# Optimization experiments

Hardware: AMD Instinct MI355X
Metric: run time of the kernel (lower is better)

The kernel has to match this reference:

```python
import jax, jax.numpy as jnp
import numpy as np

NUM_NODES = 2048
EMB = (512, 512, 256)
LATENT = 512
N_FEAT = 512
N_TOTAL = 16384  # batch_size * NUM_NODES
N_EDGES = 524288


def setup_inputs() -> dict:
    key = jax.random.key(0)
    ks = jax.random.split(key, 14)
    s = 0.02
    inp = {
        "x": jax.random.normal(ks[0], (N_TOTAL, N_FEAT), jnp.float32),
        "edge_index": jax.random.randint(ks[1], (2, N_EDGES), 0, N_TOTAL, dtype=jnp.int64),
        "batch_size": 8,
        "batch_index": jax.random.randint(ks[2], (N_TOTAL,), 0, 8, dtype=jnp.int64),
        "W1": jax.random.normal(ks[3], (N_FEAT, EMB[0]), jnp.float32) * s,
        "b1": jnp.zeros((EMB[0],), jnp.float32),
        "W2": jax.random.normal(ks[4], (EMB[0], EMB[1]), jnp.float32) * s,
        "b2": jnp.zeros((EMB[1],), jnp.float32),
        "W3": jax.random.normal(ks[5], (EMB[1], EMB[2]), jnp.float32) * s,
        "b3": jnp.zeros((EMB[2],), jnp.float32),
        "We": jax.random.normal(ks[6], (NUM_NODES * EMB[2], LATENT), jnp.float32) * s,
        "be": jnp.zeros((LATENT,), jnp.float32),
        "Wd": jax.random.normal(ks[7], (LATENT, NUM_NODES), jnp.float32) * s,
        "bd": jnp.zeros((NUM_NODES,), jnp.float32),
    }
    return inp


def reference(x, edge_index, batch_size, batch_index, W1, b1, W2, b2, W3, b3, We, be, Wd, bd):
    N = x.shape[0]
    loops = jnp.arange(N)
    row = jnp.concatenate([edge_index[0], loops])  # sources
    col = jnp.concatenate([edge_index[1], loops])  # targets
    # symmetric degree normalization (PyG GCNConv with self loops)
    deg = jax.ops.segment_sum(jnp.ones_like(col, dtype=x.dtype), col, num_segments=N)
    dinv = jnp.where(deg > 0, jax.lax.rsqrt(deg), jnp.zeros_like(deg))
    norm = (dinv[row] * dinv[col])[:, None]  # [E+N, 1]

    def gcn(h, W, b):
        h = h @ W  # transform first (PyG order)
        return jax.ops.segment_sum(h[row] * norm, col, num_segments=N) + b

    h = jax.nn.relu(gcn(x, W1, b1))
    h = jax.nn.relu(gcn(h, W2, b2))
    h = gcn(h, W3, b3)                      # [N, EMB[2]]
    h = h.reshape(-1, NUM_NODES * EMB[2])   # [batch, NUM_NODES*EMB[2]]
    z = h @ We + be                          # encoder Linear
    out = z @ Wd + bd                        # decoder Linear -> [batch, NUM_NODES]
    return out
```

## Files before the change

kernel.cpp:

```cpp
#include <hip/hip_runtime.h>
#include <stdint.h>

#define NT 16384
#define NN 2048
#define NB 8
#define NBKT 16

typedef __attribute__((ext_vector_type(4))) float f32x4;
typedef __attribute__((ext_vector_type(8))) short s16x8;
typedef __attribute__((ext_vector_type(4))) short s16x4;

__device__ __forceinline__ float bf2f(short u) {
    unsigned v = ((unsigned)(unsigned short)u) << 16;
    return __builtin_bit_cast(float, v);
}
__device__ __forceinline__ short f2bf(float f) {
    unsigned u = __builtin_bit_cast(unsigned, f);
    u += 0x7fffu + ((u >> 16) & 1u);
    return (short)(u >> 16);
}
__device__ __forceinline__ void gload16(const void* g, void* l) {
    __builtin_amdgcn_global_load_lds(
        (const __attribute__((address_space(1))) void*)g,
        (__attribute__((address_space(3))) void*)l, 16, 0, 0);
}
__device__ __forceinline__ long long eidx(const void* ei, long long i, int is64) {
    if (is64) return ((const long long*)ei)[i];
    return (long long)((const int*)ei)[i];
}

__global__ void k_init(const void* ei, int* flag, int* cnt16) {
    if (blockIdx.x == 64) {
        __shared__ int bad;
        if (threadIdx.x == 0) bad = 0;
        __syncthreads();
        const long long* p = (const long long*)ei;
        for (int i = threadIdx.x; i < 2048; i += 256) {
            long long v = p[i];
            if (v < 0 || v >= NT) bad = 1;
        }
        __syncthreads();
        if (threadIdx.x == 0) *flag = bad ? 0 : 1;
    } else {
        int base = blockIdx.x * 4096 + threadIdx.x;
#pragma unroll
        for (int q = 0; q < 16; q++) cnt16[base + q * 256] = 0;
    }
}

__global__ void k_count16(const void* ei, int E, const int* flag, int* cnt16) {
    int e = blockIdx.x * 256 + threadIdx.x;
    if (e >= E) return;
    int f = *flag;
    int r = (int)eidx(ei, e, f);
    int c = (int)eidx(ei, (long long)E + e, f);
    atomicAdd(&cnt16[c * NBKT + (r >> 10)], 1);
}

__global__ void k_deg(const int* __restrict__ cnt16, int* __restrict__ deg) {
    int n = blockIdx.x * 256 + threadIdx.x;
    const int* p = cnt16 + n * NBKT;
    int s = 0;
#pragma unroll
    for (int j = 0; j < NBKT; j++) s += p[j];
    deg[n] = s;
}

__global__ __launch_bounds__(1024) void k_scan(const int* __restrict__ count,
        int* __restrict__ offs, float* __restrict__ dinv) {
    __shared__ int ps[1024];
    const int t = threadIdx.x;
    const int base = t * 16;
    int loc[16];
    int s = 0;
#pragma unroll
    for (int j = 0; j < 16; j++) { loc[j] = count[base + j]; s += loc[j]; }
    ps[t] = s;
    __syncthreads();
    for (int o = 1; o < 1024; o <<= 1) {
        int v = (t >= o) ? ps[t - o] : 0;
        __syncthreads();
        ps[t] += v;
        __syncthreads();
    }
    int ex = ps[t] - s;
#pragma unroll
    for (int j = 0; j < 16; j++) {
        offs[base + j] = ex;
        ex += loc[j];
        dinv[base + j] = rsqrtf((float)(loc[j] + 1));
    }
}

__global__ void k_bcur(const int* __restrict__ cnt16, const int* __restrict__ offs,
                       int* __restrict__ bcur) {
    int n = blockIdx.x * 256 + threadIdx.x;
    int running = offs[n];
#pragma unroll
    for (int b = 0; b < NBKT; b++) {
        bcur[n * NBKT + b] = running;
        running += cnt16[n * NBKT + b];
    }
}

__global__ void k_fill16(const void* ei, int E, const int* flag,
                         int* bcur, int* csr) {
    int e = blockIdx.x * 256 + threadIdx.x;
    if (e >= E) return;
    int f = *flag;
    int r = (int)eidx(ei, e, f);
    int c = (int)eidx(ei, (long long)E + e, f);
    int pos = atomicAdd(&bcur[c * NBKT + (r >> 10)], 1);
    csr[pos] = r;
}

__global__ void k_convscale(const float* __restrict__ W1, const float* __restrict__ W2,
                            const float* __restrict__ W3, short* __restrict__ Wt1,
                            short* __restrict__ Wt2, short* __restrict__ Wt3,
                            const float* __restrict__ x, const float* __restrict__ dinv,
                            short* __restrict__ xs) {
    if (blockIdx.x < 8192) {
        int i = blockIdx.x * 256 + threadIdx.x;
        f32x4 v = *(const f32x4*)(x + (size_t)i * 4);
        float d = dinv[i >> 7];
        s16x4 o;
#pragma unroll
        for (int j = 0; j < 4; j++) o[j] = f2bf(v[j] * d);
        *(s16x4*)(xs + (size_t)i * 4) = o;
    } else {
        int idx = (blockIdx.x - 8192) * 256 + threadIdx.x;
        const float* W; short* Wt; int N, base;
        if (idx < 262144)      { W = W1; Wt = Wt1; N = 512; base = idx; }
        else if (idx < 524288) { W = W2; Wt = Wt2; N = 512; base = idx - 262144; }
        else                   { W = W3; Wt = Wt3; N = 256; base = idx - 524288; }
        int k = base / N, n = base - k * N;
        Wt[(size_t)n * 512 + k] = f2bf(W[base]);
    }
}

__global__ __launch_bounds__(256, 4) void k_gemm(const short* __restrict__ A,
        const short* __restrict__ Bt, short* __restrict__ Co, int N, int K) {
    __shared__ short As[64 * 64];
    __shared__ short Bs[128 * 64];
    const int t = threadIdx.x;
    const int w = t >> 6, l = t & 63;
    const int row0 = blockIdx.x * 64;
    const int col0 = blockIdx.y * 128;
    const int lr = l & 15, lhi = l >> 4;
    const int wc = w * 32;
    f32x4 acc[4][2] = {};
    int arow[2], ajs[2], brow[4], bjs[4];
#pragma unroll
    for (int i = 0; i < 2; i++) {
        int s = t + i * 256;
        arow[i] = s >> 3; ajs[i] = (s & 7) ^ (arow[i] & 7);
    }
#pragma unroll
    for (int i = 0; i < 4; i++) {
        int s = t + i * 256;
        brow[i] = s >> 3; bjs[i] = (s & 7) ^ (brow[i] & 7);
    }
    int aoff[2][4], boff[2][2];
#pragma unroll
    for (int kk = 0; kk < 2; kk++) {
#pragma unroll
        for (int m = 0; m < 4; m++) {
            int ar = m * 16 + lr;
            aoff[kk][m] = ar * 64 + (((kk * 4 + lhi) ^ (ar & 7)) << 3);
        }
#pragma unroll
        for (int n = 0; n < 2; n++) {
            int br = wc + n * 16 + lr;
            boff[kk][n] = br * 64 + (((kk * 4 + lhi) ^ (br & 7)) << 3);
        }
    }
    for (int k0 = 0; k0 < K; k0 += 64) {
#pragma unroll
        for (int i = 0; i < 2; i++)
            gload16(A + (size_t)(row0 + arow[i]) * K + k0 + ajs[i] * 8,
                    (void*)(As + (t + i * 256) * 8));
#pragma unroll
        for (int i = 0; i < 4; i++)
            gload16(Bt + (size_t)(col0 + brow[i]) * K + k0 + bjs[i] * 8,
                    (void*)(Bs + (t + i * 256) * 8));
        __syncthreads();
#pragma unroll
        for (int kk = 0; kk < 2; kk++) {
            s16x8 af[4], bfr[2];
#pragma unroll
            for (int m = 0; m < 4; m++) af[m]  = *(const s16x8*)(As + aoff[kk][m]);
#pragma unroll
            for (int n = 0; n < 2; n++) bfr[n] = *(const s16x8*)(Bs + boff[kk][n]);
#pragma unroll
            for (int m = 0; m < 4; m++)
#pragma unroll
                for (int n = 0; n < 2; n++)
                    acc[m][n] = __builtin_amdgcn_mfma_f32_16x16x32_bf16(af[m], bfr[n], acc[m][n], 0, 0, 0);
        }
        __syncthreads();
    }
#pragma unroll
    for (int m = 0; m < 4; m++)
#pragma unroll
        for (int n = 0; n < 2; n++)
#pragma unroll
            for (int j = 0; j < 4; j++) {
                int r = row0 + m * 16 + lhi * 4 + j;
                int c = col0 + wc + n * 16 + lr;
                Co[(size_t)r * N + c] = f2bf(acc[m][n][j]);
            }
}

__global__ __launch_bounds__(256) void k_agg512(const short* __restrict__ T,
        const int* __restrict__ offs, const int* __restrict__ cnt,
        const int* __restrict__ csr, const float* __restrict__ dinv,
        const float* __restrict__ bias, short* __restrict__ H) {
    const int w = threadIdx.x >> 6, l = threadIdx.x & 63;
    const int node = blockIdx.x * 4 + w;
    const int c0 = l * 8;
    const short* base = T + c0;
    float acc[8];
    {
        s16x8 r = *(const s16x8*)(base + (size_t)node * 512);
#pragma unroll
        for (int v = 0; v < 8; v++) acc[v] = bf2f(r[v]);
    }
    const int beg = offs[node], end = beg + cnt[node];
    int j = beg;
    for (; j + 8 <= end; j += 8) {
        int sIx[8];
#pragma unroll
        for (int q = 0; q < 8; q++) sIx[q] = csr[j + q];
        s16x8 r[8];
#pragma unroll
        for (int q = 0; q < 8; q++) r[q] = *(const s16x8*)(base + (size_t)sIx[q] * 512);
#pragma unroll
        for (int v = 0; v < 8; v++) {
            float s01 = bf2f(r[0][v]) + bf2f(r[1][v]);
            float s23 = bf2f(r[2][v]) + bf2f(r[3][v]);
            float s45 = bf2f(r[4][v]) + bf2f(r[5][v]);
            float s67 = bf2f(r[6][v]) + bf2f(r[7][v]);
            acc[v] += (s01 + s23) + (s45 + s67);
        }
    }
    for (; j + 2 <= end; j += 2) {
        int s0 = csr[j], s1 = csr[j + 1];
        s16x8 r0 = *(const s16x8*)(base + (size_t)s0 * 512);
        s16x8 r1 = *(const s16x8*)(base + (size_t)s1 * 512);
#pragma unroll
        for (int v = 0; v < 8; v++) acc[v] += bf2f(r0[v]) + bf2f(r1[v]);
    }
    for (; j < end; j++) {
        s16x8 r0 = *(const s16x8*)(base + (size_t)csr[j] * 512);
#pragma unroll
        for (int v = 0; v < 8; v++) acc[v] += bf2f(r0[v]);
    }
    const float dc = dinv[node];
    f32x4 b0 = *(const f32x4*)(bias + c0);
    f32x4 b1 = *(const f32x4*)(bias + c0 + 4);
    s16x8 outv;
#pragma unroll
    for (int v = 0; v < 8; v++) {
        float bb = (v < 4) ? b0[v] : b1[v - 4];
        float o = acc[v] * dc + bb;
        o = fmaxf(o, 0.f);
        o *= dc;
        outv[v] = f2bf(o);
    }
    *(s16x8*)(H + (size_t)node * 512 + c0) = outv;
}

__global__ __launch_bounds__(256) void k_enc(const short* __restrict__ T,
        const int* __restrict__ offs, const int* __restrict__ cnt,
        const int* __restrict__ csr, const float* __restrict__ dinv,
        const float* __restrict__ b3, const float* __restrict__ We,
        float* __restrict__ part) {
    __shared__ float hB[8 * 512];
    __shared__ float red[32 * 128];
    const int t = threadIdx.x;
    const int w = t >> 6, l = t & 63;
    const int ln0 = blockIdx.x * 2;
    const int c0 = l * 4;
    const short* base = T + c0;
    f32x4 bb = *(const f32x4*)(b3 + c0);
    for (int p = 0; p < 4; p++) {
        const int i = w * 4 + p;
        const int b = i >> 1, lnk = i & 1;
        const int node = b * NN + ln0 + lnk;
        float acc[4];
        {
            s16x4 r = *(const s16x4*)(base + (size_t)node * 256);
#pragma unroll
            for (int v = 0; v < 4; v++) acc[v] = bf2f(r[v]);
        }
        const int beg = offs[node], end = beg + cnt[node];
        int j = beg;
        for (; j + 8 <= end; j += 8) {
            int sIx[8];
#pragma unroll
            for (int q = 0; q < 8; q++) sIx[q] = csr[j + q];
            s16x4 r[8];
#pragma unroll
            for (int q = 0; q < 8; q++) r[q] = *(const s16x4*)(base + (size_t)sIx[q] * 256);
#pragma unroll
            for (int v = 0; v < 4; v++) {
                float s01 = bf2f(r[0][v]) + bf2f(r[1][v]);
                float s23 = bf2f(r[2][v]) + bf2f(r[3][v]);
                float s45 = bf2f(r[4][v]) + bf2f(r[5][v]);
                float s67 = bf2f(r[6][v]) + bf2f(r[7][v]);
                acc[v] += (s01 + s23) + (s45 + s67);
            }
        }
        for (; j < end; j++) {
            s16x4 r0 = *(const s16x4*)(base + (size_t)csr[j] * 256);
#pragma unroll
            for (int v = 0; v < 4; v++) acc[v] += bf2f(r0[v]);
        }
        const float dc = dinv[node];
        f32x4 o;
#pragma unroll
        for (int v = 0; v < 4; v++) o[v] = acc[v] * dc + bb[v];
        *(f32x4*)(&hB[b * 512 + lnk * 256 + c0]) = o;
    }
    __syncthreads();
    const int col = (t & 127) * 4;
    const int khalf = t >> 7;
    float acc[8][4] = {};
    const float* wp = We + (size_t)(blockIdx.x * 512 + khalf * 256) * 512 + col;
    const float* hp = hB + khalf * 256;
#pragma unroll 2
    for (int k = 0; k < 256; k++) {
        f32x4 wv = *(const f32x4*)(wp + (size_t)k * 512);
        float h0 = hp[k],        h1 = hp[512 + k],  h2 = hp[1024 + k], h3v = hp[1536 + k];
        float h4 = hp[2048 + k], h5 = hp[2560 + k], h6 = hp[3072 + k], h7 = hp[3584 + k];
#pragma unroll
        for (int c = 0; c < 4; c++) {
            acc[0][c] += h0 * wv[c];
            acc[1][c] += h1 * wv[c];
            acc[2][c] += h2 * wv[c];
            acc[3][c] += h3v * wv[c];
            acc[4][c] += h4 * wv[c];
            acc[5][c] += h5 * wv[c];
            acc[6][c] += h6 * wv[c];
            acc[7][c] += h7 * wv[c];
        }
    }
    if (khalf) {
#pragma unroll
        for (int b = 0; b < 8; b++)
#pragma unroll
            for (int c = 0; c < 4; c++)
                red[(b * 4 + c) * 128 + (t - 128)] = acc[b][c];
    }
    __syncthreads();
    if (!khalf) {
#pragma unroll
        for (int b = 0; b < 8; b++) {
            f32x4 o;
#pragma unroll
            for (int c = 0; c < 4; c++) o[c] = acc[b][c] + red[(b * 4 + c) * 128 + t];
            *(f32x4*)(part + (size_t)blockIdx.x * 4096 + b * 512 + col) = o;
        }
    }
}

__global__ __launch_bounds__(256) void k_zred(const float* __restrict__ part,
                                              float* __restrict__ zpart) {
    const int n = blockIdx.x * 256 + threadIdx.x;
    const int p0 = blockIdx.y * 128;
    float s = 0.f;
    for (int q = 0; q < 128; q++) s += part[(size_t)(p0 + q) * 4096 + n];
    zpart[(size_t)blockIdx.y * 4096 + n] = s;
}

__global__ __launch_bounds__(256) void k_dec(const float* __restrict__ zpart,
        const float* __restrict__ be, const float* __restrict__ Wd,
        const float* __restrict__ bd, float* __restrict__ out) {
    __shared__ float zs[512];
    const int b = blockIdx.x >> 3;
    const int n = ((blockIdx.x & 7) << 8) + threadIdx.x;
    for (int i = threadIdx.x; i < 512; i += 256) {
        float s = be[i];
#pragma unroll
        for (int p = 0; p < 8; p++) s += zpart[(size_t)p * 4096 + b * 512 + i];
        zs[i] = s;
    }
    __syncthreads();
    float acc = bd[n];
    for (int k = 0; k < 512; k++) acc += zs[k] * Wd[(size_t)k * 2048 + n];
    out[b * 2048 + n] = acc;
}

extern "C" void kernel_launch(void* const* d_in, const int* in_sizes, int n_in,
                              void* d_out, int out_size, void* d_ws, size_t ws_size,
                              hipStream_t stream) {
    const float* x  = (const float*)d_in[0];
    const void*  ei = d_in[1];
    const float* W1 = (const float*)d_in[4];
    const float* b1 = (const float*)d_in[5];
    const float* W2 = (const float*)d_in[6];
    const float* b2 = (const float*)d_in[7];
    const float* W3 = (const float*)d_in[8];
    const float* b3 = (const float*)d_in[9];
    const float* We = (const float*)d_in[10];
    const float* be = (const float*)d_in[11];
    const float* Wd = (const float*)d_in[12];
    const float* bd = (const float*)d_in[13];
    float* out = (float*)d_out;
    const int E = in_sizes[1] / 2;

    char* ws = (char*)d_ws;
    size_t off = 0;
    auto alloc = [&](size_t bytes) {
        void* p = ws + off;
        off = (off + bytes + 255) & ~(size_t)255;
        return p;
    };
    int*   flag   = (int*)  alloc(4);
    int*   deg    = (int*)  alloc((size_t)NT * 4);
    int*   offs   = (int*)  alloc((size_t)NT * 4);
    float* dinv   = (float*)alloc((size_t)NT * 4);
    int*   csr    = (int*)  alloc((size_t)E * 4);
    short* Wt1    = (short*)alloc((size_t)512 * 512 * 2);
    short* Wt2    = (short*)alloc((size_t)512 * 512 * 2);
    short* Wt3    = (short*)alloc((size_t)256 * 512 * 2);
    short* bufA   = (short*)alloc((size_t)NT * 512 * 2);
    short* bufB   = (short*)alloc((size_t)NT * 512 * 2);
    float* part   = (float*)alloc((size_t)1024 * 4096 * 4);
    float* zpart  = (float*)alloc((size_t)8 * 4096 * 4);
    int*   cnt16  = (int*)part;
    int*   bcur   = ((int*)part) + NT * NBKT;

    k_init<<<65, 256, 0, stream>>>(ei, flag, cnt16);
    k_count16<<<(E + 255) / 256, 256, 0, stream>>>(ei, E, flag, cnt16);
    k_deg<<<NT / 256, 256, 0, stream>>>(cnt16, deg);
    k_scan<<<1, 1024, 0, stream>>>(deg, offs, dinv);
    k_bcur<<<NT / 256, 256, 0, stream>>>(cnt16, offs, bcur);
    k_fill16<<<(E + 255) / 256, 256, 0, stream>>>(ei, E, flag, bcur, csr);

    k_convscale<<<10752, 256, 0, stream>>>(W1, W2, W3, Wt1, Wt2, Wt3, x, dinv, bufA);

    dim3 g1(256, 4);
    k_gemm<<<g1, 256, 0, stream>>>(bufA, Wt1, bufB, 512, 512);
    k_agg512<<<NT / 4, 256, 0, stream>>>(bufB, offs, deg, csr, dinv, b1, bufA);
    k_gemm<<<g1, 256, 0, stream>>>(bufA, Wt2, bufB, 512, 512);
    k_agg512<<<NT / 4, 256, 0, stream>>>(bufB, offs, deg, csr, dinv, b2, bufA);
    dim3 g3(256, 2);
    k_gemm<<<g3, 256, 0, stream>>>(bufA, Wt3, bufB, 256, 512);

    k_enc<<<1024, 256, 0, stream>>>(bufB, offs, deg, csr, dinv, b3, We, part);
    dim3 gz(16, 8);
    k_zred<<<gz, 256, 0, stream>>>(part, zpart);
    k_dec<<<64, 256, 0, stream>>>(zpart, be, Wd, bd, out);
}
```

Baseline: 493.2 us.

## Split 512-wide aggregation into two 256-channel passes for cache locality

The gather-aggregate kernel now handles half the feature channels per launch, with a channel offset argument, and is launched twice per layer. Each pass touches only a 256-channel (512-byte) slice of every source row, so the gathered working set halves and more of it may stay in L2/MALL across random neighbor accesses. In exchange there are twice as many launches, the CSR indices and degrees are re-read per pass, and each lane does narrower 8-byte loads.

After: 485.0 us. No clear change (-1.7%).

```diff
diff --git a/kernel.cpp b/kernel.cpp
--- a/kernel.cpp
+++ b/kernel.cpp
@@ -211,19 +211,19 @@
             }
 }
 
-__global__ __launch_bounds__(256) void k_agg512(const short* __restrict__ T,
+__global__ __launch_bounds__(256) void k_agg512h(const short* __restrict__ T,
         const int* __restrict__ offs, const int* __restrict__ cnt,
         const int* __restrict__ csr, const float* __restrict__ dinv,
-        const float* __restrict__ bias, short* __restrict__ H) {
+        const float* __restrict__ bias, short* __restrict__ H, int choff) {
     const int w = threadIdx.x >> 6, l = threadIdx.x & 63;
     const int node = blockIdx.x * 4 + w;
-    const int c0 = l * 8;
+    const int c0 = choff + l * 4;
     const short* base = T + c0;
-    float acc[8];
+    float acc[4];
     {
-        s16x8 r = *(const s16x8*)(base + (size_t)node * 512);
-#pragma unroll
-        for (int v = 0; v < 8; v++) acc[v] = bf2f(r[v]);
+        s16x4 r = *(const s16x4*)(base + (size_t)node * 512);
+#pragma unroll
+        for (int v = 0; v < 4; v++) acc[v] = bf2f(r[v]);
     }
     const int beg = offs[node], end = beg + cnt[node];
     int j = beg;
@@ -231,11 +231,11 @@
         int sIx[8];
 #pragma unroll
         for (int q = 0; q < 8; q++) sIx[q] = csr[j + q];
-        s16x8 r[8];
-#pragma unroll
-        for (int q = 0; q < 8; q++) r[q] = *(const s16x8*)(base + (size_t)sIx[q] * 512);
-#pragma unroll
-        for (int v = 0; v < 8; v++) {
+        s16x4 r[8];
+#pragma unroll
+        for (int q = 0; q < 8; q++) r[q] = *(const s16x4*)(base + (size_t)sIx[q] * 512);
+#pragma unroll
+        for (int v = 0; v < 4; v++) {
             float s01 = bf2f(r[0][v]) + bf2f(r[1][v]);
             float s23 = bf2f(r[2][v]) + bf2f(r[3][v]);
             float s45 = bf2f(r[4][v]) + bf2f(r[5][v]);
@@ -245,29 +245,27 @@
     }
     for (; j + 2 <= end; j += 2) {
         int s0 = csr[j], s1 = csr[j + 1];
-        s16x8 r0 = *(const s16x8*)(base + (size_t)s0 * 512);
-        s16x8 r1 = *(const s16x8*)(base + (size_t)s1 * 512);
-#pragma unroll
-        for (int v = 0; v < 8; v++) acc[v] += bf2f(r0[v]) + bf2f(r1[v]);
+        s16x4 r0 = *(const s16x4*)(base + (size_t)s0 * 512);
+        s16x4 r1 = *(const s16x4*)(base + (size_t)s1 * 512);
+#pragma unroll
+        for (int v = 0; v < 4; v++) acc[v] += bf2f(r0[v]) + bf2f(r1[v]);
     }
     for (; j < end; j++) {
-        s16x8 r0 = *(const s16x8*)(base + (size_t)csr[j] * 512);
-#pragma unroll
-        for (int v = 0; v < 8; v++) acc[v] += bf2f(r0[v]);
+        s16x4 r0 = *(const s16x4*)(base + (size_t)csr[j] * 512);
+#pragma unroll
+        for (int v = 0; v < 4; v++) acc[v] += bf2f(r0[v]);
     }
     const float dc = dinv[node];
-    f32x4 b0 = *(const f32x4*)(bias + c0);
-    f32x4 b1 = *(const f32x4*)(bias + c0 + 4);
-    s16x8 outv;
-#pragma unroll
-    for (int v = 0; v < 8; v++) {
-        float bb = (v < 4) ? b0[v] : b1[v - 4];
-        float o = acc[v] * dc + bb;
+    f32x4 bb = *(const f32x4*)(bias + c0);
+    s16x4 outv;
+#pragma unroll
+    for (int v = 0; v < 4; v++) {
+        float o = acc[v] * dc + bb[v];
         o = fmaxf(o, 0.f);
         o *= dc;
         outv[v] = f2bf(o);
     }
-    *(s16x8*)(H + (size_t)node * 512 + c0) = outv;
+    *(s16x4*)(H + (size_t)node * 512 + c0) = outv;
 }
 
 __global__ __launch_bounds__(256) void k_enc(const short* __restrict__ T,
@@ -442,9 +440,11 @@
 
     dim3 g1(256, 4);
     k_gemm<<<g1, 256, 0, stream>>>(bufA, Wt1, bufB, 512, 512);
-    k_agg512<<<NT / 4, 256, 0, stream>>>(bufB, offs, deg, csr, dinv, b1, bufA);
+    k_agg512h<<<NT / 4, 256, 0, stream>>>(bufB, offs, deg, csr, dinv, b1, bufA, 0);
+    k_agg512h<<<NT / 4, 256, 0, stream>>>(bufB, offs, deg, csr, dinv, b1, bufA, 256);
     k_gemm<<<g1, 256, 0, stream>>>(bufA, Wt2, bufB, 512, 512);
-    k_agg512<<<NT / 4, 256, 0, stream>>>(bufB, offs, deg, csr, dinv, b2, bufA);
+    k_agg512h<<<NT / 4, 256, 0, stream>>>(bufB, offs, deg, csr, dinv, b2, bufA, 0);
+    k_agg512h<<<NT / 4, 256, 0, stream>>>(bufB, offs, deg, csr, dinv, b2, bufA, 256);
     dim3 g3(256, 2);
     k_gemm<<<g3, 256, 0, stream>>>(bufA, Wt3, bufB, 256, 512);
 
```
